# Performance work log

Measured on AMD Instinct MI355X. Metric: run time of the kernel, lower is better.

Reference implementation:

```python
import jax, jax.numpy as jnp
import numpy as np

N_WL = 296      # spectral points after dropping last 4
POOL = 4
FM = N_WL // POOL  # 74
HEAD = 64
EMB = 48


def setup_inputs() -> dict:
    key = jax.random.key(0)
    ks = jax.random.split(key, 16)
    B = 2048
    inp = {
        "x": jax.random.uniform(ks[0], (B, 300), dtype=jnp.float32),
        # FeaturePicker DI
        "wDI": jax.random.normal(ks[1], (HEAD, FM, FM), dtype=jnp.float32),
        "bDI": jax.random.normal(ks[2], (HEAD,), dtype=jnp.float32),
        "fcDI_w": jax.random.normal(ks[3], (EMB, HEAD), dtype=jnp.float32) * 0.1,
        "fcDI_b": jax.random.normal(ks[4], (EMB,), dtype=jnp.float32) * 0.1,
        # FeaturePicker NDI
        "wNDI": jax.random.normal(ks[5], (HEAD, FM, FM), dtype=jnp.float32),
        "bNDI": jax.random.normal(ks[6], (HEAD,), dtype=jnp.float32),
        "fcNDI_w": jax.random.normal(ks[7], (EMB, HEAD), dtype=jnp.float32) * 0.1,
        "fcNDI_b": jax.random.normal(ks[8], (EMB,), dtype=jnp.float32) * 0.1,
        # head MLP
        "fc1_w": jax.random.normal(ks[9], (48, 96), dtype=jnp.float32) * 0.1,
        "fc1_b": jax.random.normal(ks[10], (48,), dtype=jnp.float32) * 0.1,
        "l1_w": jax.random.normal(ks[11], (20, 48), dtype=jnp.float32) * 0.1,
        "l1_b": jax.random.normal(ks[12], (20,), dtype=jnp.float32) * 0.1,
        "l2_w": jax.random.normal(ks[13], (1, 20), dtype=jnp.float32) * 0.1,
        "l2_b": jax.random.normal(ks[14], (1,), dtype=jnp.float32) * 0.1,
    }
    return inp


def _feature_picker(m, wmap, bias, fw, fb):
    # m: [B, 296, 296] -> avgpool 4x4 -> [B, 74, 74]
    B = m.shape[0]
    p = m.reshape(B, FM, POOL, FM, POOL).mean(axis=(2, 4))
    # weighted sum against each of HEAD weight maps (== [B,5476] @ [5476,HEAD])
    h = jnp.einsum('bij,hij->bh', p, wmap) + bias
    h = jax.nn.elu(h)
    return jax.nn.elu(h @ fw.T + fb)  # [B, EMB]


def reference(x, wDI, bDI, fcDI_w, fcDI_b, wNDI, bNDI, fcNDI_w, fcNDI_b,
              fc1_w, fc1_b, l1_w, l1_b, l2_w, l2_b):
    x0 = x[:, :-4]                       # [B, 296]
    a = x0[:, None, :]                   # unsqueeze(1)
    b = x0[:, :, None]                   # unsqueeze(2)
    DI = a - b                           # [B, 296, 296]
    NDI = (a - b) / (a + b + 1e-5)
    eDI = _feature_picker(DI, wDI, bDI, fcDI_w, fcDI_b)
    eNDI = _feature_picker(NDI, wNDI, bNDI, fcNDI_w, fcNDI_b)
    emb = jnp.concatenate([eDI, eNDI], axis=1)      # [B, 96]
    emb = jax.nn.elu(emb @ fc1_w.T + fc1_b)
    emb = jax.nn.elu(emb @ l1_w.T + l1_b)
    return jax.nn.sigmoid(emb @ l2_w.T + l2_b)      # [B, 1]
```

## Files before the change

kernel.cpp:

```cpp
#include <hip/hip_runtime.h>
#include <hip/hip_bf16.h>
#include <math.h>

#define NWL    296
#define FMD    74
#define HEAD   64
#define EMBD   48
#define BATCH  2048
#define XCOLS  300
#define NPAIR  2701
#define NPAIR_P 3072
#define KSPLIT 8
#define SEGLEN (NPAIR_P / KSPLIT)
#define MR     8

#define WS_CMR  0
#define WS_PAIR (FMD * HEAD)
#define WS_WATT (WS_PAIR + NPAIR_P)
#define WS_PNDI (WS_WATT + HEAD * NPAIR_P / 2)

typedef _Float16 f16x8 __attribute__((ext_vector_type(8)));
typedef _Float16 f16x2 __attribute__((ext_vector_type(2)));
typedef float f32x4 __attribute__((ext_vector_type(4)));

__device__ __forceinline__ float eluf(float x) { return x > 0.f ? x : expm1f(x); }

__device__ __forceinline__ float ratio_sum16(float4 uv, float4 vv) {
  float u2[4] = { fmaf(2.f, uv.x, 1e-5f), fmaf(2.f, uv.y, 1e-5f),
                  fmaf(2.f, uv.z, 1e-5f), fmaf(2.f, uv.w, 1e-5f) };
  float u[4]  = { uv.x, uv.y, uv.z, uv.w };
  float v[4]  = { vv.x, vv.y, vv.z, vv.w };
  float s = 0.f;
  #pragma unroll
  for (int a = 0; a < 4; a++) {
    float va = v[a] + 1e-5f;
    #pragma unroll
    for (int b = 0; b < 4; b++)
      s = fmaf(u2[b], __builtin_amdgcn_rcpf(u[b] + va), s);
  }
  return s - 16.f;
}

__device__ __forceinline__ void pair_decode(int k, int& I, int& J) {
  I = (int)((147.0f - sqrtf(21609.0f - 8.0f * (float)k)) * 0.5f);
  int base = (I * (147 - I)) >> 1;
  while (base > k) { I--; base = (I * (147 - I)) >> 1; }
  while (I < 72 && ((I + 1) * (146 - I)) / 2 <= k) { I++; base = (I * (147 - I)) >> 1; }
  J = I + 1 + (k - base);
}

__global__ __launch_bounds__(256) void fcr_prep_v7(
    const float* __restrict__ wDI,
    const float* __restrict__ wNDI,
    float* __restrict__ ws) {
  __shared__ float wdL[FMD * FMD];
  __shared__ float wnL[FMD * FMD];

  int t = threadIdx.x;
  int h = blockIdx.x;

  const float4* gd = (const float4*)(wDI + (size_t)h * FMD * FMD);
  const float4* gn = (const float4*)(wNDI + (size_t)h * FMD * FMD);
  for (int i = t; i < FMD * FMD / 4; i += 256) {
    ((float4*)wdL)[i] = gd[i];
    ((float4*)wnL)[i] = gn[i];
  }
  __syncthreads();

  _Float16* wATt = (_Float16*)(ws + WS_WATT);
  for (int k = t; k < NPAIR_P; k += 256) {
    float v = 0.f;
    if (k < NPAIR) {
      int I, J; pair_decode(k, I, J);
      v = (wnL[I * FMD + J] - wnL[J * FMD + I]) * 0.0625f;
    }
    wATt[(size_t)h * NPAIR_P + k] = (_Float16)v;
  }

  if (t < FMD) {
    int K = t;
    float cs = 0.f, rs = 0.f;
    for (int I = 0; I < FMD; I++) {
      cs += wdL[I * FMD + K];
      rs += wdL[K * FMD + I];
    }
    ws[WS_CMR + K * 64 + h] = cs - rs;
  }

  if (h == 0) {
    unsigned* P = (unsigned*)(ws + WS_PAIR);
    for (int k = t; k < NPAIR_P; k += 256) {
      unsigned pb = 0;
      if (k < NPAIR) {
        int I, J; pair_decode(k, I, J);
        pb = (unsigned)(4 * I) | ((unsigned)(4 * J) << 16);
      }
      P[k] = pb;
    }
  }
}

__global__ __launch_bounds__(256, 6) void fcr_main_v7(
    const float* __restrict__ x,
    float* __restrict__ ws) {
  __shared__ float xs[MR][308];
  __shared__ _Float16 Sm[MR][392];
  __shared__ unsigned pairsL[SEGLEN];

  const unsigned* pairG = (const unsigned*)(ws + WS_PAIR);
  const _Float16* wATt = (const _Float16*)(ws + WS_WATT);
  float* pNDI = ws + WS_PNDI;

  int t = threadIdx.x;
  int seg = blockIdx.x & (KSPLIT - 1);
  int row0 = (blockIdx.x >> 3) * MR;
  int k0 = seg * SEGLEN;

  for (int i = t; i < MR * (NWL / 4); i += 256) {
    int r = i / (NWL / 4), c4 = i - r * (NWL / 4);
    *(float4*)&xs[r][4 * c4] = *(const float4*)(x + (size_t)(row0 + r) * XCOLS + 4 * c4);
  }
  for (int i = t; i < SEGLEN; i += 256) pairsL[i] = pairG[k0 + i];
  __syncthreads();

  int mA = t & 7;
  int kg = t >> 3;
  #pragma unroll
  for (int j = 0; j < SEGLEN / 64; j++) {
    int kc = 2 * kg + 64 * j;
    uint2 pb2 = *(const uint2*)&pairsL[kc];
    int bI0 = pb2.x & 0xFFFF, bJ0 = pb2.x >> 16;
    int bI1 = pb2.y & 0xFFFF, bJ1 = pb2.y >> 16;
    float4 u0 = *(const float4*)&xs[mA][bJ0];
    float4 v0 = *(const float4*)&xs[mA][bI0];
    float4 u1 = *(const float4*)&xs[mA][bJ1];
    float4 v1 = *(const float4*)&xs[mA][bI1];
    float s0 = ratio_sum16(u0, v0);
    float s1 = ratio_sum16(u1, v1);
    f16x2 pk = { (_Float16)s0, (_Float16)s1 };
    *(f16x2*)&Sm[mA][kc] = pk;
  }
  __syncthreads();

  int lane = t & 63;
  int wv   = t >> 6;
  int n_in = lane & 15;
  int quad = lane >> 4;
  int h    = wv * 16 + n_in;
  f32x4 acc = {0.f, 0.f, 0.f, 0.f};
  #pragma unroll
  for (int c = 0; c < SEGLEN / 32; c++) {
    f16x8 aF = *(const f16x8*)&Sm[n_in & 7][c * 32 + quad * 8];
    f16x8 bF = *(const f16x8*)&wATt[(size_t)h * NPAIR_P + k0 + c * 32 + quad * 8];
    acc = __builtin_amdgcn_mfma_f32_16x16x32_f16(aF, bF, acc, 0, 0, 0);
  }

  if (quad < 2) {
    #pragma unroll
    for (int r = 0; r < 4; r++) {
      int m = quad * 4 + r;
      pNDI[((size_t)seg * BATCH + row0 + m) * 64 + h] = acc[r];
    }
  }
}

__global__ __launch_bounds__(256) void fcr_tail_v7(
    const float* __restrict__ x,
    const float* __restrict__ ws,
    const float* __restrict__ bDI,
    const float* __restrict__ fcDI_w,
    const float* __restrict__ fcDI_b,
    const float* __restrict__ bNDI,
    const float* __restrict__ fcNDI_w,
    const float* __restrict__ fcNDI_b,
    const float* __restrict__ fc1_w,
    const float* __restrict__ fc1_b,
    const float* __restrict__ l1_w,
    const float* __restrict__ l1_b,
    const float* __restrict__ l2_w,
    const float* __restrict__ l2_b,
    float* __restrict__ out) {
  __shared__ float xs[MR][308];
  __shared__ float xs4[MR][FMD];
  __shared__ _Float16 wDT[HEAD * EMBD];
  __shared__ _Float16 wNT[HEAD * EMBD];
  __shared__ _Float16 w1T[96 * 48];
  __shared__ _Float16 wl1T[48 * 20];
  __shared__ float wl2s[20];
  __shared__ float bDs[HEAD], bNs[HEAD], bDe[EMBD], bNe[EMBD], b1[48], bl1s[20];
  __shared__ float bl2s;
  __shared__ float ehD[MR][68], ehN[MR][68];
  __shared__ float e2[MR][100];
  __shared__ float e3[MR][52];
  __shared__ float e4[MR][20];

  const float* cmr  = ws + WS_CMR;
  const float* pNDI = ws + WS_PNDI;

  int t = threadIdx.x;
  int row0 = blockIdx.x * MR;

  for (int i = t; i < MR * (NWL / 4); i += 256) {
    int r = i / (NWL / 4), c4 = i - r * (NWL / 4);
    *(float4*)&xs[r][4 * c4] = *(const float4*)(x + (size_t)(row0 + r) * XCOLS + 4 * c4);
  }
  for (int i = t; i < HEAD * EMBD; i += 256) {
    int o = i >> 6, hh = i & 63;
    wDT[hh * EMBD + o] = (_Float16)fcDI_w[i];
    wNT[hh * EMBD + o] = (_Float16)fcNDI_w[i];
  }
  for (int i = t; i < 48 * 96; i += 256) {
    int o = i / 96, j = i - o * 96;
    w1T[j * 48 + o] = (_Float16)fc1_w[i];
  }
  for (int i = t; i < 20 * 48; i += 256) {
    int o = i / 48, j = i - o * 48;
    wl1T[j * 20 + o] = (_Float16)l1_w[i];
  }
  if (t < 20)   { wl2s[t] = l2_w[t]; bl1s[t] = l1_b[t]; }
  if (t < HEAD) { bDs[t] = bDI[t]; bNs[t] = bNDI[t]; }
  if (t < EMBD) { bDe[t] = fcDI_b[t]; bNe[t] = fcNDI_b[t]; }
  if (t < 48)   b1[t] = fc1_b[t];
  if (t == 0)   bl2s = l2_b[0];
  __syncthreads();

  for (int i = t; i < MR * FMD; i += 256) {
    int r = i / FMD, K = i - r * FMD;
    xs4[r][K] = 0.25f * (xs[r][4*K] + xs[r][4*K+1] + xs[r][4*K+2] + xs[r][4*K+3]);
  }
  __syncthreads();

  {
    int hh = t & 63, g = t >> 6;
    float d0 = 0.f, d1 = 0.f;
    for (int K = 0; K < FMD; K++) {
      float w = cmr[K * 64 + hh];
      d0 = fmaf(xs4[2*g][K],   w, d0);
      d1 = fmaf(xs4[2*g+1][K], w, d1);
    }
    ehD[2*g][hh]   = eluf(d0 + bDs[hh]);
    ehD[2*g+1][hh] = eluf(d1 + bDs[hh]);
  }
  for (int i = t; i < MR * HEAD; i += 256) {
    int r = i >> 6, hh = i & 63;
    int row = row0 + r;
    float hN = bNs[hh];
    for (int s2 = 0; s2 < KSPLIT; s2++)
      hN += pNDI[((size_t)s2 * BATCH + row) * 64 + hh];
    ehN[r][hh] = eluf(hN);
  }
  __syncthreads();

  for (int i = t; i < MR * 96; i += 256) {
    int r = i / 96, o = i - r * 96;
    int isN = o >= 48;
    int o2 = isN ? o - 48 : o;
    const _Float16* wb = isN ? wNT : wDT;
    const float* eb = isN ? &ehN[r][0] : &ehD[r][0];
    float s = isN ? bNe[o2] : bDe[o2];
    for (int hh = 0; hh < 64; hh++)
      s = fmaf(eb[hh], (float)wb[hh * EMBD + o2], s);
    e2[r][o] = eluf(s);
  }
  __syncthreads();

  for (int i = t; i < MR * 48; i += 256) {
    int r = i / 48, o = i - r * 48;
    float s = b1[o];
    for (int j = 0; j < 96; j++)
      s = fmaf(e2[r][j], (float)w1T[j * 48 + o], s);
    e3[r][o] = eluf(s);
  }
  __syncthreads();

  if (t < MR * 20) {
    int r = t / 20, o = t - r * 20;
    float s = bl1s[o];
    for (int j = 0; j < 48; j++)
      s = fmaf(e3[r][j], (float)wl1T[j * 20 + o], s);
    e4[r][o] = eluf(s);
  }
  __syncthreads();

  if (t < MR) {
    float s = bl2s;
    for (int j = 0; j < 20; j++)
      s = fmaf(e4[t][j], wl2s[j], s);
    out[row0 + t] = 1.f / (1.f + expf(-s));
  }
}

extern "C" void kernel_launch(void* const* d_in, const int* in_sizes, int n_in,
                              void* d_out, int out_size, void* d_ws, size_t ws_size,
                              hipStream_t stream) {
  const float* x      = (const float*)d_in[0];
  const float* wDI    = (const float*)d_in[1];
  const float* bDI    = (const float*)d_in[2];
  const float* fcDI_w = (const float*)d_in[3];
  const float* fcDI_b = (const float*)d_in[4];
  const float* wNDI   = (const float*)d_in[5];
  const float* bNDI   = (const float*)d_in[6];
  const float* fcNDI_w= (const float*)d_in[7];
  const float* fcNDI_b= (const float*)d_in[8];
  const float* fc1_w  = (const float*)d_in[9];
  const float* fc1_b  = (const float*)d_in[10];
  const float* l1_w   = (const float*)d_in[11];
  const float* l1_b   = (const float*)d_in[12];
  const float* l2_w   = (const float*)d_in[13];
  const float* l2_b   = (const float*)d_in[14];
  float* out = (float*)d_out;
  float* ws = (float*)d_ws;

  fcr_prep_v7<<<HEAD, 256, 0, stream>>>(wDI, wNDI, ws);
  fcr_main_v7<<<(BATCH / MR) * KSPLIT, 256, 0, stream>>>(x, ws);
  fcr_tail_v7<<<BATCH / MR, 256, 0, stream>>>(x, ws, bDI, fcDI_w, fcDI_b,
      bNDI, fcNDI_w, fcNDI_b, fc1_w, fc1_b, l1_w, l1_b, l2_w, l2_b, out);
}
```

Before: 127.0 us.

## Fuse tail MLP into main kernel via last-block-wins atomic counter

Removes the separate tail kernel. The last of the split-K blocks for each row block, found with an atomic counter, reduces the partial NDI sums and runs the MLP head inline. The fp16 conversion of the MLP weights moves into the prep kernel, so per-block transposing into shared memory goes away. Shared memory is aliased into one buffer and the occupancy hint drops from 6 to 4, which may reduce latency hiding in the main compute.

After: 202.2 us. 1.59x slower.

```diff
diff --git a/kernel.cpp b/kernel.cpp
--- a/kernel.cpp
+++ b/kernel.cpp
@@ -13,11 +13,17 @@
 #define KSPLIT 8
 #define SEGLEN (NPAIR_P / KSPLIT)
 #define MR     8
+#define ROWBLKS (BATCH / MR)
 
 #define WS_CMR  0
 #define WS_PAIR (FMD * HEAD)
 #define WS_WATT (WS_PAIR + NPAIR_P)
 #define WS_PNDI (WS_WATT + HEAD * NPAIR_P / 2)
+#define WS_CNT  (WS_PNDI + KSPLIT * BATCH * HEAD)
+#define WS_WD16 (WS_CNT + ROWBLKS)
+#define WS_WN16 (WS_WD16 + 1536)
+#define WS_W116 (WS_WN16 + 1536)
+#define WS_WL16 (WS_W116 + 2304)
 
 typedef _Float16 f16x8 __attribute__((ext_vector_type(8)));
 typedef _Float16 f16x2 __attribute__((ext_vector_type(2)));
@@ -49,9 +55,13 @@
   J = I + 1 + (k - base);
 }
 
-__global__ __launch_bounds__(256) void fcr_prep_v7(
+__global__ __launch_bounds__(256) void fcr_prep_v8(
     const float* __restrict__ wDI,
     const float* __restrict__ wNDI,
+    const float* __restrict__ fcDI_w,
+    const float* __restrict__ fcNDI_w,
+    const float* __restrict__ fc1_w,
+    const float* __restrict__ l1_w,
     float* __restrict__ ws) {
   __shared__ float wdL[FMD * FMD];
   __shared__ float wnL[FMD * FMD];
@@ -97,23 +107,57 @@
       }
       P[k] = pb;
     }
-  }
-}
-
-__global__ __launch_bounds__(256, 6) void fcr_main_v7(
+  } else if (h == 1) {
+    unsigned* cnt = (unsigned*)(ws + WS_CNT);
+    if (t < ROWBLKS) cnt[t] = 0u;
+  } else if (h == 2) {
+    _Float16* w16 = (_Float16*)(ws + WS_WD16);
+    for (int i = t; i < EMBD * HEAD; i += 256) w16[i] = (_Float16)fcDI_w[i];
+  } else if (h == 3) {
+    _Float16* w16 = (_Float16*)(ws + WS_WN16);
+    for (int i = t; i < EMBD * HEAD; i += 256) w16[i] = (_Float16)fcNDI_w[i];
+  } else if (h == 4) {
+    _Float16* w16 = (_Float16*)(ws + WS_W116);
+    for (int i = t; i < 48 * 96; i += 256) w16[i] = (_Float16)fc1_w[i];
+  } else if (h == 5) {
+    _Float16* w16 = (_Float16*)(ws + WS_WL16);
+    for (int i = t; i < 20 * 48; i += 256) w16[i] = (_Float16)l1_w[i];
+  }
+}
+
+__global__ __launch_bounds__(256, 4) void fcr_main_v8(
     const float* __restrict__ x,
-    float* __restrict__ ws) {
-  __shared__ float xs[MR][308];
-  __shared__ _Float16 Sm[MR][392];
-  __shared__ unsigned pairsL[SEGLEN];
+    float* __restrict__ ws,
+    const float* __restrict__ bDI,
+    const float* __restrict__ fcDI_b,
+    const float* __restrict__ bNDI,
+    const float* __restrict__ fcNDI_b,
+    const float* __restrict__ fc1_b,
+    const float* __restrict__ l1_b,
+    const float* __restrict__ l2_w,
+    const float* __restrict__ l2_b,
+    float* __restrict__ out) {
+  __shared__ __align__(16) char smem[17664];
+  __shared__ int winS;
+  float (*xs)[308]       = (float (*)[308])(smem);
+  _Float16 (*Sm)[392]    = (_Float16 (*)[392])(smem + 9856);
+  unsigned* pairsL       = (unsigned*)(smem + 16128);
+  float (*xs4)[FMD]      = (float (*)[FMD])(smem + 9856);
+  float (*e2)[96]        = (float (*)[96])(smem + 12224);
+  float (*e3)[48]        = (float (*)[48])(smem + 15296);
+  float (*e4)[20]        = (float (*)[20])(smem + 16832);
+  float (*ehD)[64]       = (float (*)[64])(smem);
+  float (*ehN)[64]       = (float (*)[64])(smem + 2048);
 
   const unsigned* pairG = (const unsigned*)(ws + WS_PAIR);
   const _Float16* wATt = (const _Float16*)(ws + WS_WATT);
   float* pNDI = ws + WS_PNDI;
+  unsigned* cnt = (unsigned*)(ws + WS_CNT);
 
   int t = threadIdx.x;
   int seg = blockIdx.x & (KSPLIT - 1);
-  int row0 = (blockIdx.x >> 3) * MR;
+  int rowblk = blockIdx.x >> 3;
+  int row0 = rowblk * MR;
   int k0 = seg * SEGLEN;
 
   for (int i = t; i < MR * (NWL / 4); i += 256) {
@@ -129,15 +173,11 @@
   for (int j = 0; j < SEGLEN / 64; j++) {
     int kc = 2 * kg + 64 * j;
     uint2 pb2 = *(const uint2*)&pairsL[kc];
-    int bI0 = pb2.x & 0xFFFF, bJ0 = pb2.x >> 16;
-    int bI1 = pb2.y & 0xFFFF, bJ1 = pb2.y >> 16;
-    float4 u0 = *(const float4*)&xs[mA][bJ0];
-    float4 v0 = *(const float4*)&xs[mA][bI0];
-    float4 u1 = *(const float4*)&xs[mA][bJ1];
-    float4 v1 = *(const float4*)&xs[mA][bI1];
-    float s0 = ratio_sum16(u0, v0);
-    float s1 = ratio_sum16(u1, v1);
-    f16x2 pk = { (_Float16)s0, (_Float16)s1 };
+    float4 u0 = *(const float4*)&xs[mA][pb2.x >> 16];
+    float4 v0 = *(const float4*)&xs[mA][pb2.x & 0xFFFF];
+    float4 u1 = *(const float4*)&xs[mA][pb2.y >> 16];
+    float4 v1 = *(const float4*)&xs[mA][pb2.y & 0xFFFF];
+    f16x2 pk = { (_Float16)ratio_sum16(u0, v0), (_Float16)ratio_sum16(u1, v1) };
     *(f16x2*)&Sm[mA][kc] = pk;
   }
   __syncthreads();
@@ -159,70 +199,25 @@
     #pragma unroll
     for (int r = 0; r < 4; r++) {
       int m = quad * 4 + r;
-      pNDI[((size_t)seg * BATCH + row0 + m) * 64 + h] = acc[r];
-    }
-  }
-}
-
-__global__ __launch_bounds__(256) void fcr_tail_v7(
-    const float* __restrict__ x,
-    const float* __restrict__ ws,
-    const float* __restrict__ bDI,
-    const float* __restrict__ fcDI_w,
-    const float* __restrict__ fcDI_b,
-    const float* __restrict__ bNDI,
-    const float* __restrict__ fcNDI_w,
-    const float* __restrict__ fcNDI_b,
-    const float* __restrict__ fc1_w,
-    const float* __restrict__ fc1_b,
-    const float* __restrict__ l1_w,
-    const float* __restrict__ l1_b,
-    const float* __restrict__ l2_w,
-    const float* __restrict__ l2_b,
-    float* __restrict__ out) {
-  __shared__ float xs[MR][308];
-  __shared__ float xs4[MR][FMD];
-  __shared__ _Float16 wDT[HEAD * EMBD];
-  __shared__ _Float16 wNT[HEAD * EMBD];
-  __shared__ _Float16 w1T[96 * 48];
-  __shared__ _Float16 wl1T[48 * 20];
-  __shared__ float wl2s[20];
-  __shared__ float bDs[HEAD], bNs[HEAD], bDe[EMBD], bNe[EMBD], b1[48], bl1s[20];
-  __shared__ float bl2s;
-  __shared__ float ehD[MR][68], ehN[MR][68];
-  __shared__ float e2[MR][100];
-  __shared__ float e3[MR][52];
-  __shared__ float e4[MR][20];
-
-  const float* cmr  = ws + WS_CMR;
-  const float* pNDI = ws + WS_PNDI;
-
-  int t = threadIdx.x;
-  int row0 = blockIdx.x * MR;
-
-  for (int i = t; i < MR * (NWL / 4); i += 256) {
-    int r = i / (NWL / 4), c4 = i - r * (NWL / 4);
-    *(float4*)&xs[r][4 * c4] = *(const float4*)(x + (size_t)(row0 + r) * XCOLS + 4 * c4);
-  }
-  for (int i = t; i < HEAD * EMBD; i += 256) {
-    int o = i >> 6, hh = i & 63;
-    wDT[hh * EMBD + o] = (_Float16)fcDI_w[i];
-    wNT[hh * EMBD + o] = (_Float16)fcNDI_w[i];
-  }
-  for (int i = t; i < 48 * 96; i += 256) {
-    int o = i / 96, j = i - o * 96;
-    w1T[j * 48 + o] = (_Float16)fc1_w[i];
-  }
-  for (int i = t; i < 20 * 48; i += 256) {
-    int o = i / 48, j = i - o * 48;
-    wl1T[j * 20 + o] = (_Float16)l1_w[i];
-  }
-  if (t < 20)   { wl2s[t] = l2_w[t]; bl1s[t] = l1_b[t]; }
-  if (t < HEAD) { bDs[t] = bDI[t]; bNs[t] = bNDI[t]; }
-  if (t < EMBD) { bDe[t] = fcDI_b[t]; bNe[t] = fcNDI_b[t]; }
-  if (t < 48)   b1[t] = fc1_b[t];
-  if (t == 0)   bl2s = l2_b[0];
-  __syncthreads();
+      __hip_atomic_store(&pNDI[((size_t)seg * BATCH + row0 + m) * 64 + h], acc[r],
+                         __ATOMIC_RELAXED, __HIP_MEMORY_SCOPE_AGENT);
+    }
+  }
+  __syncthreads();
+
+  if (t == 0) {
+    unsigned old = __hip_atomic_fetch_add(&cnt[rowblk], 1u,
+                      __ATOMIC_ACQ_REL, __HIP_MEMORY_SCOPE_AGENT);
+    winS = (old == KSPLIT - 1);
+  }
+  __syncthreads();
+  if (!winS) return;
+
+  const float* cmr = ws + WS_CMR;
+  const _Float16* wD16 = (const _Float16*)(ws + WS_WD16);
+  const _Float16* wN16 = (const _Float16*)(ws + WS_WN16);
+  const _Float16* w116 = (const _Float16*)(ws + WS_W116);
+  const _Float16* wL16 = (const _Float16*)(ws + WS_WL16);
 
   for (int i = t; i < MR * FMD; i += 256) {
     int r = i / FMD, K = i - r * FMD;
@@ -238,15 +233,18 @@
       d0 = fmaf(xs4[2*g][K],   w, d0);
       d1 = fmaf(xs4[2*g+1][K], w, d1);
     }
-    ehD[2*g][hh]   = eluf(d0 + bDs[hh]);
-    ehD[2*g+1][hh] = eluf(d1 + bDs[hh]);
+    float bv = bDI[hh];
+    ehD[2*g][hh]   = eluf(d0 + bv);
+    ehD[2*g+1][hh] = eluf(d1 + bv);
   }
   for (int i = t; i < MR * HEAD; i += 256) {
     int r = i >> 6, hh = i & 63;
     int row = row0 + r;
-    float hN = bNs[hh];
+    float hN = bNDI[hh];
+    #pragma unroll
     for (int s2 = 0; s2 < KSPLIT; s2++)
-      hN += pNDI[((size_t)s2 * BATCH + row) * 64 + hh];
+      hN += __hip_atomic_load(&pNDI[((size_t)s2 * BATCH + row) * 64 + hh],
+                              __ATOMIC_RELAXED, __HIP_MEMORY_SCOPE_AGENT);
     ehN[r][hh] = eluf(hN);
   }
   __syncthreads();
@@ -255,37 +253,51 @@
     int r = i / 96, o = i - r * 96;
     int isN = o >= 48;
     int o2 = isN ? o - 48 : o;
-    const _Float16* wb = isN ? wNT : wDT;
-    const float* eb = isN ? &ehN[r][0] : &ehD[r][0];
-    float s = isN ? bNe[o2] : bDe[o2];
-    for (int hh = 0; hh < 64; hh++)
-      s = fmaf(eb[hh], (float)wb[hh * EMBD + o2], s);
+    const _Float16* wrow = (isN ? wN16 : wD16) + o2 * 64;
+    const float* eb = isN ? ehN[r] : ehD[r];
+    float s = isN ? fcNDI_b[o2] : fcDI_b[o2];
+    #pragma unroll
+    for (int c = 0; c < 8; c++) {
+      f16x8 wvv = *(const f16x8*)(wrow + c * 8);
+      #pragma unroll
+      for (int j = 0; j < 8; j++) s = fmaf((float)wvv[j], eb[c * 8 + j], s);
+    }
     e2[r][o] = eluf(s);
   }
   __syncthreads();
 
   for (int i = t; i < MR * 48; i += 256) {
     int r = i / 48, o = i - r * 48;
-    float s = b1[o];
-    for (int j = 0; j < 96; j++)
-      s = fmaf(e2[r][j], (float)w1T[j * 48 + o], s);
+    const _Float16* wrow = w116 + o * 96;
+    float s = fc1_b[o];
+    #pragma unroll
+    for (int c = 0; c < 12; c++) {
+      f16x8 wvv = *(const f16x8*)(wrow + c * 8);
+      #pragma unroll
+      for (int j = 0; j < 8; j++) s = fmaf((float)wvv[j], e2[r][c * 8 + j], s);
+    }
     e3[r][o] = eluf(s);
   }
   __syncthreads();
 
   if (t < MR * 20) {
     int r = t / 20, o = t - r * 20;
-    float s = bl1s[o];
-    for (int j = 0; j < 48; j++)
-      s = fmaf(e3[r][j], (float)wl1T[j * 20 + o], s);
+    const _Float16* wrow = wL16 + o * 48;
+    float s = l1_b[o];
+    #pragma unroll
+    for (int c = 0; c < 6; c++) {
+      f16x8 wvv = *(const f16x8*)(wrow + c * 8);
+      #pragma unroll
+      for (int j = 0; j < 8; j++) s = fmaf((float)wvv[j], e3[r][c * 8 + j], s);
+    }
     e4[r][o] = eluf(s);
   }
   __syncthreads();
 
   if (t < MR) {
-    float s = bl2s;
+    float s = l2_b[0];
     for (int j = 0; j < 20; j++)
-      s = fmaf(e4[t][j], wl2s[j], s);
+      s = fmaf(e4[t][j], l2_w[j], s);
     out[row0 + t] = 1.f / (1.f + expf(-s));
   }
 }
@@ -311,8 +323,7 @@
   float* out = (float*)d_out;
   float* ws = (float*)d_ws;
 
-  fcr_prep_v7<<<HEAD, 256, 0, stream>>>(wDI, wNDI, ws);
-  fcr_main_v7<<<(BATCH / MR) * KSPLIT, 256, 0, stream>>>(x, ws);
-  fcr_tail_v7<<<BATCH / MR, 256, 0, stream>>>(x, ws, bDI, fcDI_w, fcDI_b,
-      bNDI, fcNDI_w, fcNDI_b, fc1_w, fc1_b, l1_w, l1_b, l2_w, l2_b, out);
-}
+  fcr_prep_v8<<<HEAD, 256, 0, stream>>>(wDI, wNDI, fcDI_w, fcNDI_w, fc1_w, l1_w, ws);
+  fcr_main_v8<<<ROWBLKS * KSPLIT, 256, 0, stream>>>(x, ws, bDI, fcDI_b,
+      bNDI, fcNDI_b, fc1_b, l1_b, l2_w, l2_b, out);
+}
```
